# Kernel tuning notes

Hardware: AMD Instinct MI355X
Metric: run time of the kernel (lower is better)

Reference implementation:

```python
import jax, jax.numpy as jnp
import numpy as np

N = 100000          # num nodes
E = 1_600_000       # num edges (avg degree 16)
IN = 512
OUT = 64
HOPS = 4


def setup_inputs() -> dict:
    key = jax.random.key(0)
    k1, k2, k3 = jax.random.split(key, 3)
    x = jax.random.normal(k1, (N, IN), dtype=jnp.float32)
    W = jax.random.normal(k2, (OUT, IN), dtype=jnp.float32) * 0.02
    b = jnp.zeros((OUT,), dtype=jnp.float32)
    edge_index = jax.random.randint(k3, (2, E), 0, N, dtype=jnp.int32)
    return {"x": x, "W": W, "b": b, "edge_index": edge_index}


def reference(x, W, b, edge_index):
    # 1) linear projection first (low-memory SGC variant)
    h = x @ W.T + b                      # [N, OUT]
    n = h.shape[0]

    # 2) gcn_norm: add self loops, symmetric D^{-1/2} A D^{-1/2}
    row, col = edge_index[0], edge_index[1]
    loop = jnp.arange(n, dtype=row.dtype)
    row = jnp.concatenate([row, loop])   # [E+N]
    col = jnp.concatenate([col, loop])
    ew = jnp.ones(row.shape[0], dtype=h.dtype)
    deg = jax.ops.segment_sum(ew, col, num_segments=n)          # in-degree incl. self loop
    dinv = jnp.where(deg > 0, jax.lax.rsqrt(deg), 0.0)
    w = dinv[row] * ew * dinv[col]       # normalized edge weights [E+N]

    # 3) hops x SpMM: adj_t built with (row=col, col=row) => out[col] += w * h[row]
    for _ in range(HOPS):
        h = jax.ops.segment_sum(w[:, None] * h[row], col, num_segments=n)
    return h
```

## Files before the change

### kernel.cpp

```cpp
#include <hip/hip_runtime.h>
#include <stdint.h>

#define IN_DIM 512
#define OUT_DIM 64

typedef short bf16x8 __attribute__((ext_vector_type(8)));
typedef float f32x4 __attribute__((ext_vector_type(4)));

__device__ inline unsigned short f2bf(float f) {
    unsigned int u = __float_as_uint(f);
    return (unsigned short)((u + 0x7FFFu + ((u >> 16) & 1u)) >> 16);
}
__device__ inline float bf2f(unsigned short s) {
    return __uint_as_float(((unsigned int)s) << 16);
}

__global__ void zero_deg_kernel(int* __restrict__ deg, int N) {
    int i = blockIdx.x * blockDim.x + threadIdx.x;
    if (i < N) deg[i] = 0;
}

__global__ __launch_bounds__(256) void hist_part_kernel(const int* __restrict__ col,
                                                        int* __restrict__ deg, int E, int N) {
    int part = blockIdx.x & 7;
    int lo = (int)((long)part * N / 8);
    int hi = (int)((long)(part + 1) * N / 8);
    int stride = (gridDim.x >> 3) * blockDim.x;
    int i = (blockIdx.x >> 3) * blockDim.x + threadIdx.x;
    for (; i < E; i += stride) {
        int c = col[i];
        if (c >= lo && c < hi) atomicAdd(&deg[c], 1);
    }
}

__global__ void dinv_kernel(const int* __restrict__ deg, float* __restrict__ dinv,
                            float* __restrict__ d2, int N) {
    int i = blockIdx.x * blockDim.x + threadIdx.x;
    if (i < N) {
        float d = (float)deg[i] + 1.0f;
        dinv[i] = 1.0f / sqrtf(d);
        d2[i] = 1.0f / d;
    }
}

__global__ void pack_w_kernel(const float* __restrict__ W,
                              unsigned short* __restrict__ Bhi,
                              unsigned short* __restrict__ Blo) {
    int tid = blockIdx.x * blockDim.x + threadIdx.x;
    if (tid >= 4096) return;
    int L = tid & 63;
    int ct = tid >> 6;
    int t = ct & 15, c = ct >> 4;
    int o = c * 16 + (L & 15);
    int k0 = t * 32 + (L >> 4) * 8;
    const float* src = W + (size_t)o * IN_DIM + k0;
    #pragma unroll
    for (int j = 0; j < 8; ++j) {
        float w = src[j];
        unsigned short h = f2bf(w);
        Bhi[(size_t)tid * 8 + j] = h;
        Blo[(size_t)tid * 8 + j] = f2bf(w - bf2f(h));
    }
}

__global__ __launch_bounds__(1024) void scan_local_kernel(const int* __restrict__ deg,
                                                          int* __restrict__ rowptr,
                                                          int* __restrict__ bsum, int N) {
    __shared__ int sm[16];
    int tid = threadIdx.x, lane = tid & 63, wid = tid >> 6;
    int i = blockIdx.x * 4096 + tid * 4;
    int4 v = make_int4(0, 0, 0, 0);
    if (i + 3 < N) {
        v = *(const int4*)(deg + i);
    } else {
        if (i < N) v.x = deg[i];
        if (i + 1 < N) v.y = deg[i + 1];
        if (i + 2 < N) v.z = deg[i + 2];
        if (i + 3 < N) v.w = deg[i + 3];
    }
    int s1 = v.x, s2 = s1 + v.y, s3 = s2 + v.z, s4 = s3 + v.w;
    int incl = s4;
    #pragma unroll
    for (int d = 1; d < 64; d <<= 1) {
        int t = __shfl_up(incl, d, 64);
        if (lane >= d) incl += t;
    }
    if (lane == 63) sm[wid] = incl;
    __syncthreads();
    if (tid == 0) {
        int run = 0;
        #pragma unroll
        for (int w2 = 0; w2 < 16; ++w2) { int t = sm[w2]; sm[w2] = run; run += t; }
        bsum[blockIdx.x] = run;
    }
    __syncthreads();
    int tbase = incl - s4 + sm[wid];
    if (i + 3 < N) {
        *(int4*)(rowptr + i) = make_int4(tbase, tbase + s1, tbase + s2, tbase + s3);
    } else {
        if (i < N)     rowptr[i]     = tbase;
        if (i + 1 < N) rowptr[i + 1] = tbase + s1;
        if (i + 2 < N) rowptr[i + 2] = tbase + s2;
        if (i + 3 < N) rowptr[i + 3] = tbase + s3;
    }
}

__global__ __launch_bounds__(1024) void scan_add_kernel(int* __restrict__ rowptr,
                                                        int* __restrict__ cursor,
                                                        const int* __restrict__ bsum,
                                                        int N, int nb) {
    __shared__ int soff;
    if (threadIdx.x == 0) {
        int off = 0;
        for (int j = 0; j < (int)blockIdx.x; ++j) off += bsum[j];
        soff = off;
        if ((int)blockIdx.x == nb - 1) {
            int tot = off;
            for (int j = blockIdx.x; j < nb; ++j) tot += bsum[j];
            rowptr[N] = tot;
        }
    }
    __syncthreads();
    int off = soff;
    int i = blockIdx.x * 4096 + threadIdx.x * 4;
    if (i + 3 < N) {
        int4 r = *(int4*)(rowptr + i);
        r.x += off; r.y += off; r.z += off; r.w += off;
        *(int4*)(rowptr + i) = r;
        *(int4*)(cursor + i) = r;
    } else {
        for (int j = 0; j < 4; ++j)
            if (i + j < N) { int r = rowptr[i + j] + off; rowptr[i + j] = r; cursor[i + j] = r; }
    }
}

__global__ __launch_bounds__(256) void fill_part_kernel(const int* __restrict__ row,
                                                        const int* __restrict__ col,
                                                        int* __restrict__ cursor,
                                                        int* __restrict__ csr, int E, int N) {
    int part = blockIdx.x & 7;
    int lo = (int)((long)part * N / 8);
    int hi = (int)((long)(part + 1) * N / 8);
    int stride = (gridDim.x >> 3) * blockDim.x;
    int i = (blockIdx.x >> 3) * blockDim.x + threadIdx.x;
    for (; i < E; i += stride) {
        int c = col[i];
        if (c >= lo && c < hi) {
            int pos = atomicAdd(&cursor[c], 1);
            csr[pos] = row[i];
        }
    }
}

__global__ __launch_bounds__(256) void mfma_gemm_kernel(const float* __restrict__ x,
                                                        const unsigned short* __restrict__ Bhi,
                                                        const unsigned short* __restrict__ Blo,
                                                        const float* __restrict__ bias,
                                                        const float* __restrict__ dinv,
                                                        float* __restrict__ h, int N) {
    int lane = threadIdx.x & 63;
    int wid  = __builtin_amdgcn_readfirstlane(threadIdx.x >> 6);
    int quad = lane >> 4, r16 = lane & 15;
    long rowBase = ((long)blockIdx.x * 4 + wid) * 32;
    if (rowBase >= N) return;
    bool full = (rowBase + 32 <= N);

    f32x4 acc[2][4];
    #pragma unroll
    for (int rt = 0; rt < 2; ++rt)
        #pragma unroll
        for (int c = 0; c < 4; ++c) acc[rt][c] = (f32x4){0.f, 0.f, 0.f, 0.f};

    int row0 = (int)rowBase + r16;
    int row1 = (int)rowBase + 16 + r16;
    int row0c = full ? row0 : (row0 < N ? row0 : N - 1);
    int row1c = full ? row1 : (row1 < N ? row1 : N - 1);
    const float* a0p = x + (size_t)row0c * IN_DIM + quad * 8;
    const float* a1p = x + (size_t)row1c * IN_DIM + quad * 8;

    for (int t = 0; t < 16; ++t) {
        bf16x8 bh[4], bl[4];
        #pragma unroll
        for (int c = 0; c < 4; ++c) {
            size_t off = ((size_t)(c * 16 + t) * 64 + lane) * 8;
            union { int4 i; bf16x8 b; } uh, ul;
            uh.i = *(const int4*)(Bhi + off);
            ul.i = *(const int4*)(Blo + off);
            bh[c] = uh.b; bl[c] = ul.b;
        }
        bf16x8 ah[2], al[2];
        #pragma unroll
        for (int rt = 0; rt < 2; ++rt) {
            const float* p = (rt ? a1p : a0p) + t * 32;
            float4 f0 = *(const float4*)p;
            float4 f1 = *(const float4*)(p + 4);
            float v[8] = {f0.x, f0.y, f0.z, f0.w, f1.x, f1.y, f1.z, f1.w};
            #pragma unroll
            for (int j = 0; j < 8; ++j) {
                unsigned short hi = f2bf(v[j]);
                ah[rt][j] = (short)hi;
                al[rt][j] = (short)f2bf(v[j] - bf2f(hi));
            }
        }
        #pragma unroll
        for (int rt = 0; rt < 2; ++rt)
            #pragma unroll
            for (int c = 0; c < 4; ++c) {
                acc[rt][c] = __builtin_amdgcn_mfma_f32_16x16x32_bf16(ah[rt], bh[c], acc[rt][c], 0, 0, 0);
                acc[rt][c] = __builtin_amdgcn_mfma_f32_16x16x32_bf16(ah[rt], bl[c], acc[rt][c], 0, 0, 0);
                acc[rt][c] = __builtin_amdgcn_mfma_f32_16x16x32_bf16(al[rt], bh[c], acc[rt][c], 0, 0, 0);
            }
    }

    float bb[4];
    #pragma unroll
    for (int c = 0; c < 4; ++c) bb[c] = bias[c * 16 + r16];
    #pragma unroll
    for (int rt = 0; rt < 2; ++rt)
        #pragma unroll
        for (int rr = 0; rr < 4; ++rr) {
            int row = (int)rowBase + rt * 16 + quad * 4 + rr;
            if (row < N) {
                float dv = dinv[row];
                #pragma unroll
                for (int c = 0; c < 4; ++c)
                    h[(size_t)row * OUT_DIM + c * 16 + r16] = dv * (acc[rt][c][rr] + bb[c]);
            }
        }
}

__global__ __launch_bounds__(256) void hop_kernel(const float* __restrict__ src,
                                                  float* __restrict__ dst,
                                                  const int* __restrict__ csr,
                                                  const int* __restrict__ rowptr,
                                                  const float* __restrict__ scale, int N) {
    int lane = threadIdx.x & 63;
    int wid = __builtin_amdgcn_readfirstlane(threadIdx.x >> 6);
    int node = blockIdx.x * 4 + wid;
    if (node >= N) return;
    float acc = src[(size_t)node * OUT_DIM + lane];
    int s = rowptr[node], e = rowptr[node + 1];
    int i = s;
    for (; i + 16 <= e; i += 16) {
        int idx[16];
        #pragma unroll
        for (int j = 0; j < 16; ++j) idx[j] = csr[i + j];
        float v[16];
        #pragma unroll
        for (int j = 0; j < 16; ++j) v[j] = src[(size_t)idx[j] * OUT_DIM + lane];
        float t0 = ((v[0] + v[1]) + (v[2] + v[3])) + ((v[4] + v[5]) + (v[6] + v[7]));
        float t1 = ((v[8] + v[9]) + (v[10] + v[11])) + ((v[12] + v[13]) + (v[14] + v[15]));
        acc += t0 + t1;
    }
    for (; i + 4 <= e; i += 4) {
        int i0 = csr[i], i1 = csr[i + 1], i2 = csr[i + 2], i3 = csr[i + 3];
        float v0 = src[(size_t)i0 * OUT_DIM + lane];
        float v1 = src[(size_t)i1 * OUT_DIM + lane];
        float v2 = src[(size_t)i2 * OUT_DIM + lane];
        float v3 = src[(size_t)i3 * OUT_DIM + lane];
        acc += (v0 + v1) + (v2 + v3);
    }
    for (; i < e; ++i) acc += src[(size_t)csr[i] * OUT_DIM + lane];
    dst[(size_t)node * OUT_DIM + lane] = scale[node] * acc;
}

extern "C" void kernel_launch(void* const* d_in, const int* in_sizes, int n_in,
                              void* d_out, int out_size, void* d_ws, size_t ws_size,
                              hipStream_t stream) {
    const float* x  = (const float*)d_in[0];
    const float* W  = (const float*)d_in[1];
    const float* b  = (const float*)d_in[2];
    const int*   ei = (const int*)d_in[3];
    int N = in_sizes[0] / IN_DIM;
    int E = in_sizes[3] / 2;
    const int* row = ei;
    const int* col = ei + E;
    float* out = (float*)d_out;

    float* dinv   = (float*)d_ws;
    float* d2     = dinv + N;
    int*   deg    = (int*)(d2 + N);
    int*   rowptr = deg + N;
    int*   cursor = rowptr + (N + 4);
    int*   bsum   = cursor + N;
    unsigned short* Bhi = (unsigned short*)(bsum + 32);
    unsigned short* Blo = Bhi + 32768;

    float* xspace = (float*)d_in[0];
    float* hbuf   = xspace;
    int*   csr    = (int*)(xspace + (size_t)N * OUT_DIM);

    dim3 blk(256);
    int gN = (N + 255) / 256;
    int gPart = 8 * 784;
    int nbScan = (N + 4095) / 4096;

    zero_deg_kernel<<<gN, blk, 0, stream>>>(deg, N);
    hist_part_kernel<<<gPart, blk, 0, stream>>>(col, deg, E, N);
    dinv_kernel<<<gN, blk, 0, stream>>>(deg, dinv, d2, N);

    pack_w_kernel<<<16, blk, 0, stream>>>(W, Bhi, Blo);

    mfma_gemm_kernel<<<(N + 127) / 128, blk, 0, stream>>>(x, Bhi, Blo, b, dinv, out, N);

    scan_local_kernel<<<nbScan, 1024, 0, stream>>>(deg, rowptr, bsum, N);
    scan_add_kernel<<<nbScan, 1024, 0, stream>>>(rowptr, cursor, bsum, N, nbScan);
    fill_part_kernel<<<gPart, blk, 0, stream>>>(row, col, cursor, csr, E, N);

    int gH = (N + 3) / 4;
    hop_kernel<<<gH, blk, 0, stream>>>(out, hbuf, csr, rowptr, d2, N);
    hop_kernel<<<gH, blk, 0, stream>>>(hbuf, out, csr, rowptr, d2, N);
    hop_kernel<<<gH, blk, 0, stream>>>(out, hbuf, csr, rowptr, d2, N);
    hop_kernel<<<gH, blk, 0, stream>>>(hbuf, out, csr, rowptr, dinv, N);
}
```

Measured before the change: 696.9 us.

## Restructure hop SpMM to use float4 gathers across 4 edge groups per wavefront

The hop kernel now has each wavefront process 8 consecutive nodes. Lanes are split into 4 groups of 16, and each lane gathers a float4 of a neighbour row, so one wavefront reads four edges at once with 128-bit loads. Partial sums are reduced across the groups with xor shuffles, and the row pointers are loaded once per chunk and broadcast by shuffle. This is meant to cut the number of load instructions and improve memory-level parallelism on the irregular gathers. In exchange it adds shuffle reductions, serialises the nodes within each wavefront, and launches fewer waves.

```diff
diff --git a/kernel.cpp b/kernel.cpp
--- a/kernel.cpp
+++ b/kernel.cpp
@@ -229,39 +229,65 @@
         }
 }
 
+#define HOP_K 8
+
 __global__ __launch_bounds__(256) void hop_kernel(const float* __restrict__ src,
                                                   float* __restrict__ dst,
                                                   const int* __restrict__ csr,
                                                   const int* __restrict__ rowptr,
                                                   const float* __restrict__ scale, int N) {
     int lane = threadIdx.x & 63;
-    int wid = __builtin_amdgcn_readfirstlane(threadIdx.x >> 6);
-    int node = blockIdx.x * 4 + wid;
-    if (node >= N) return;
-    float acc = src[(size_t)node * OUT_DIM + lane];
-    int s = rowptr[node], e = rowptr[node + 1];
-    int i = s;
-    for (; i + 16 <= e; i += 16) {
-        int idx[16];
-        #pragma unroll
-        for (int j = 0; j < 16; ++j) idx[j] = csr[i + j];
-        float v[16];
-        #pragma unroll
-        for (int j = 0; j < 16; ++j) v[j] = src[(size_t)idx[j] * OUT_DIM + lane];
-        float t0 = ((v[0] + v[1]) + (v[2] + v[3])) + ((v[4] + v[5]) + (v[6] + v[7]));
-        float t1 = ((v[8] + v[9]) + (v[10] + v[11])) + ((v[12] + v[13]) + (v[14] + v[15]));
-        acc += t0 + t1;
-    }
-    for (; i + 4 <= e; i += 4) {
-        int i0 = csr[i], i1 = csr[i + 1], i2 = csr[i + 2], i3 = csr[i + 3];
-        float v0 = src[(size_t)i0 * OUT_DIM + lane];
-        float v1 = src[(size_t)i1 * OUT_DIM + lane];
-        float v2 = src[(size_t)i2 * OUT_DIM + lane];
-        float v3 = src[(size_t)i3 * OUT_DIM + lane];
-        acc += (v0 + v1) + (v2 + v3);
-    }
-    for (; i < e; ++i) acc += src[(size_t)csr[i] * OUT_DIM + lane];
-    dst[(size_t)node * OUT_DIM + lane] = scale[node] * acc;
+    int wid  = __builtin_amdgcn_readfirstlane(threadIdx.x >> 6);
+    int g    = lane >> 4;
+    int l16  = lane & 15;
+    int w  = blockIdx.x * 4 + wid;
+    int n0 = w * HOP_K;
+    if (n0 >= N) return;
+    int nK = (N - n0 < HOP_K) ? (N - n0) : HOP_K;
+
+    int rpv = 0;
+    if (lane <= nK) rpv = rowptr[n0 + lane];
+
+    for (int j = 0; j < nK; ++j) {
+        int n = n0 + j;
+        int s = __shfl(rpv, j, 64);
+        int e = __shfl(rpv, j + 1, 64);
+
+        f32x4 self4;
+        if (lane < 16) self4 = *(const f32x4*)(src + (size_t)n * OUT_DIM + l16 * 4);
+
+        f32x4 acc = (f32x4){0.f, 0.f, 0.f, 0.f};
+        int i = s;
+        for (; i + 16 <= e; i += 16) {
+            int base = i + 4 * g;
+            int i0 = csr[base], i1 = csr[base + 1], i2 = csr[base + 2], i3 = csr[base + 3];
+            f32x4 v0 = *(const f32x4*)(src + (size_t)i0 * OUT_DIM + l16 * 4);
+            f32x4 v1 = *(const f32x4*)(src + (size_t)i1 * OUT_DIM + l16 * 4);
+            f32x4 v2 = *(const f32x4*)(src + (size_t)i2 * OUT_DIM + l16 * 4);
+            f32x4 v3 = *(const f32x4*)(src + (size_t)i3 * OUT_DIM + l16 * 4);
+            acc += (v0 + v1) + (v2 + v3);
+        }
+        for (; i + 4 <= e; i += 4) {
+            int i0 = csr[i + g];
+            acc += *(const f32x4*)(src + (size_t)i0 * OUT_DIM + l16 * 4);
+        }
+        if (i + g < e) {
+            int i0 = csr[i + g];
+            acc += *(const f32x4*)(src + (size_t)i0 * OUT_DIM + l16 * 4);
+        }
+        #pragma unroll
+        for (int d = 16; d < 64; d <<= 1) {
+            acc.x += __shfl_xor(acc.x, d, 64);
+            acc.y += __shfl_xor(acc.y, d, 64);
+            acc.z += __shfl_xor(acc.z, d, 64);
+            acc.w += __shfl_xor(acc.w, d, 64);
+        }
+        if (lane < 16) {
+            float sc = scale[n];
+            f32x4 r = (acc + self4) * sc;
+            *(f32x4*)(dst + (size_t)n * OUT_DIM + l16 * 4) = r;
+        }
+    }
 }
 
 extern "C" void kernel_launch(void* const* d_in, const int* in_sizes, int n_in,
@@ -307,7 +333,8 @@
     scan_add_kernel<<<nbScan, 1024, 0, stream>>>(rowptr, cursor, bsum, N, nbScan);
     fill_part_kernel<<<gPart, blk, 0, stream>>>(row, col, cursor, csr, E, N);
 
-    int gH = (N + 3) / 4;
+    int chunks = (N + HOP_K - 1) / HOP_K;
+    int gH = (chunks + 3) / 4;
     hop_kernel<<<gH, blk, 0, stream>>>(out, hbuf, csr, rowptr, d2, N);
     hop_kernel<<<gH, blk, 0, stream>>>(hbuf, out, csr, rowptr, d2, N);
     hop_kernel<<<gH, blk, 0, stream>>>(out, hbuf, csr, rowptr, d2, N);
```

New measurement: 715.2 us. +2.6%, slower.
